# Optimization experiments

Hardware: AMD Instinct MI355X
Metric: run time of the kernel (lower is better)

## Reference

```python
import jax, jax.numpy as jnp
import numpy as np

T, N, E = 32, 5000, 80000
F_IN, H, HD, NH, C = 128, 128, 512, 8, 10
DH = H // NH  # head dim
EPS = 1e-5


def _gcn_conv(x, src, dst, W, b):
    n = x.shape[0]
    loops = jnp.arange(n, dtype=src.dtype)
    s = jnp.concatenate([src, loops])
    d = jnp.concatenate([dst, loops])
    deg = jax.ops.segment_sum(jnp.ones_like(d, x.dtype), d, num_segments=n)
    dinv = jnp.where(deg > 0, jax.lax.rsqrt(deg), 0.0)
    h = x @ W  # [n, H]
    norm = dinv[s] * dinv[d]  # [e]
    out = jax.ops.segment_sum(h[s] * norm[:, None], d, num_segments=n)
    return out + b


def _graph_embed(x, ei, W0, b0, W1, b1, W2, b2):
    src, dst = ei[0], ei[1]
    h = jnp.tanh(_gcn_conv(x, src, dst, W0, b0))
    h = jnp.tanh(_gcn_conv(h, src, dst, W1, b1))
    h = jnp.tanh(_gcn_conv(h, src, dst, W2, b2))
    return jnp.sum(h, axis=0)  # SumAggregation over all nodes -> [H]


def _forward(x, edge_index, W0, b0, W1, b1, W2, b2,
             Wq, bq, Wk, bk, Wv, bv, Wo, bo,
             g2, beta2, Wm1, bm1, Wm2, bm2, Wl, bl):
    # per-graph GCN stack + sum aggregation -> [T, H]
    z = jax.vmap(_graph_embed, in_axes=(0, 0) + (None,) * 6)(
        x, edge_index, W0, b0, W1, b1, W2, b2)

    # unbatched multihead self-attention over the T sequence
    q = (z @ Wq + bq).reshape(T, NH, DH)
    k = (z @ Wk + bk).reshape(T, NH, DH)
    v = (z @ Wv + bv).reshape(T, NH, DH)
    scores = jnp.einsum('thd,shd->hts', q, k) / jnp.sqrt(jnp.asarray(DH, z.dtype))
    attn = jax.nn.softmax(scores, axis=-1)
    o = jnp.einsum('hts,shd->thd', attn, v).reshape(T, H)
    x_attend = o @ Wo + bo  # dropout1 is identity in eval
    # NOTE: layer_norm1 output is dead code in the original forward (assigned to x, never used)

    mlp = jax.nn.relu(x_attend @ Wm1 + bm1) @ Wm2 + bm2
    x_attend = x_attend + mlp  # dropout2 identity in eval

    mu = jnp.mean(x_attend, axis=-1, keepdims=True)
    var = jnp.var(x_attend, axis=-1, keepdims=True)
    x_attend = (x_attend - mu) * jax.lax.rsqrt(var + EPS) * g2 + beta2

    pooled = jnp.sum(jax.nn.relu(x_attend), axis=0)  # [H]
    return pooled @ Wl + bl  # [C]


def setup_inputs() -> dict:
    key = jax.random.key(0)
    ks = jax.random.split(key, 24)

    def lin(k, fan_in, shape):
        return jax.random.normal(k, shape, jnp.float32) / np.sqrt(fan_in)

    inp = {
        'x': jax.random.normal(ks[0], (T, N, F_IN), jnp.float32),
        'edge_index': jax.random.randint(ks[1], (T, 2, E), 0, N, jnp.int32),
        'W0': lin(ks[2], F_IN, (F_IN, H)), 'b0': jnp.zeros((H,), jnp.float32),
        'W1': lin(ks[3], H, (H, H)), 'b1': jnp.zeros((H,), jnp.float32),
        'W2': lin(ks[4], H, (H, H)), 'b2': jnp.zeros((H,), jnp.float32),
        'Wq': lin(ks[5], H, (H, H)), 'bq': jnp.zeros((H,), jnp.float32),
        'Wk': lin(ks[6], H, (H, H)), 'bk': jnp.zeros((H,), jnp.float32),
        'Wv': lin(ks[7], H, (H, H)), 'bv': jnp.zeros((H,), jnp.float32),
        'Wo': lin(ks[8], H, (H, H)), 'bo': jnp.zeros((H,), jnp.float32),
        'g2': jnp.ones((H,), jnp.float32), 'beta2': jnp.zeros((H,), jnp.float32),
        'Wm1': lin(ks[9], H, (H, HD)), 'bm1': jnp.zeros((HD,), jnp.float32),
        'Wm2': lin(ks[10], HD, (HD, H)), 'bm2': jnp.zeros((H,), jnp.float32),
        'Wl': lin(ks[11], H, (H, C)), 'bl': jnp.zeros((C,), jnp.float32),
    }
    return inp


def reference(x, edge_index, W0, b0, W1, b1, W2, b2,
              Wq, bq, Wk, bk, Wv, bv, Wo, bo,
              g2, beta2, Wm1, bm1, Wm2, bm2, Wl, bl):
    return _forward(x, edge_index, W0, b0, W1, b1, W2, b2,
                    Wq, bq, Wk, bk, Wv, bv, Wo, bo,
                    g2, beta2, Wm1, bm1, Wm2, bm2, Wl, bl)
```

## Files before the change

### kernel.cpp

```cpp
#include <hip/hip_runtime.h>
#include <cstdint>

#define T_ 32
#define N_ 5000
#define E_ 80000
#define H_ 128
#define HD_ 512
#define C_ 10

typedef _Float16 f16;
typedef f16 f16x8 __attribute__((ext_vector_type(8)));
typedef f16 f16x4 __attribute__((ext_vector_type(4)));
typedef f16 f16x2 __attribute__((ext_vector_type(2)));
typedef float f32x4 __attribute__((ext_vector_type(4)));

#define LDA 136
#define LDH 136
#define NB_ 8
#define EPS_ (E_ / NB_)
#define NBLK_ 313
#define GEMMB 768

__device__ inline float fast_tanh(float x) {
    return 1.0f - 2.0f / (__expf(2.0f * x) + 1.0f);
}

__device__ inline f16x8 cvt8(float4 a, float4 b) {
    return (f16x8){(f16)a.x, (f16)a.y, (f16)a.z, (f16)a.w,
                   (f16)b.x, (f16)b.y, (f16)b.z, (f16)b.w};
}

__global__ __launch_bounds__(256) void k_count(const int* __restrict__ ei, int* __restrict__ part) {
    __shared__ int cnt[N_];
    int blk = blockIdx.x;
    int t = blk & 31, seg = blk >> 5;
    int tid = threadIdx.x;
    for (int i = tid; i < N_; i += 256) cnt[i] = 0;
    __syncthreads();
    const int* dst = ei + (size_t)t * 2 * E_ + E_ + seg * EPS_;
    for (int e = tid * 4; e < EPS_; e += 1024) {
        int4 d = *(const int4*)&dst[e];
        atomicAdd(&cnt[d.x], 1);
        atomicAdd(&cnt[d.y], 1);
        atomicAdd(&cnt[d.z], 1);
        atomicAdd(&cnt[d.w], 1);
    }
    __syncthreads();
    int* p = part + (t * NB_ + seg) * N_;
    for (int i = tid * 4; i < N_; i += 1024) *(int4*)&p[i] = *(const int4*)&cnt[i];
}

__global__ __launch_bounds__(256) void k_scan(int* __restrict__ part, int* __restrict__ ptr,
                                              float* __restrict__ dinv, float* __restrict__ z) {
    __shared__ int cnt[N_];
    __shared__ int red[256];
    int t = blockIdx.x, tid = threadIdx.x;
    int base = t * N_;
    if (tid < 128) z[t * 128 + tid] = 0.0f;
    int* pp = part + t * NB_ * N_;

    for (int i = tid; i < N_; i += 256) {
        int c = 0;
#pragma unroll
        for (int s = 0; s < NB_; ++s) c += pp[s * N_ + i];
        cnt[i] = c;
        dinv[base + i] = rsqrtf((float)(c + 1));
    }
    __syncthreads();

    int vals[20];
    int sum = 0;
#pragma unroll
    for (int j = 0; j < 20; ++j) {
        int i = tid * 20 + j;
        int c = (i < N_) ? cnt[i] : 0;
        vals[j] = sum;
        sum += c;
    }
    red[tid] = sum;
    __syncthreads();
    for (int off = 1; off < 256; off <<= 1) {
        int v = (tid >= off) ? red[tid - off] : 0;
        __syncthreads();
        red[tid] += v;
        __syncthreads();
    }
    int prev = (tid > 0) ? red[tid - 1] : 0;
#pragma unroll
    for (int j = 0; j < 20; ++j) {
        int i = tid * 20 + j;
        if (i < N_) cnt[i] = prev + vals[j];
    }
    __syncthreads();

    for (int i = tid; i < N_; i += 256) {
        int run = cnt[i];
        ptr[base + i] = run;
#pragma unroll
        for (int s = 0; s < NB_; ++s) {
            int c = pp[s * N_ + i];
            pp[s * N_ + i] = run;
            run += c;
        }
    }
}

__global__ __launch_bounds__(256) void k_scatter(const int* __restrict__ ei,
                                                 const int* __restrict__ part,
                                                 uint16_t* __restrict__ col) {
    __shared__ int cur[N_];
    int blk = blockIdx.x;
    int t = blk & 31, seg = blk >> 5;
    int tid = threadIdx.x;
    const int* off = part + (t * NB_ + seg) * N_;
    for (int i = tid * 4; i < N_; i += 1024) *(int4*)&cur[i] = *(const int4*)&off[i];
    __syncthreads();
    const int* src = ei + (size_t)t * 2 * E_ + seg * EPS_;
    const int* dst = src + E_;
    uint16_t* cl = col + (size_t)t * E_;
    for (int e = tid * 4; e < EPS_; e += 1024) {
        int4 s4 = *(const int4*)&src[e];
        int4 d4 = *(const int4*)&dst[e];
        cl[atomicAdd(&cur[d4.x], 1)] = (uint16_t)s4.x;
        cl[atomicAdd(&cur[d4.y], 1)] = (uint16_t)s4.y;
        cl[atomicAdd(&cur[d4.z], 1)] = (uint16_t)s4.z;
        cl[atomicAdd(&cur[d4.w], 1)] = (uint16_t)s4.w;
    }
}

__global__ __launch_bounds__(256) void k_wprep(const float* __restrict__ W0,
                                               const float* __restrict__ W1,
                                               const float* __restrict__ W2,
                                               f16* __restrict__ Wt) {
    const float* W = (blockIdx.x == 0) ? W0 : (blockIdx.x == 1) ? W1 : W2;
    f16* dst = Wt + blockIdx.x * 16384;
    for (int idx = threadIdx.x; idx < 16384; idx += 256) {
        int c = idx >> 7, k = idx & 127;
        dst[idx] = (f16)W[k * 128 + c];
    }
}

template <bool F32IN>
__global__ __launch_bounds__(256, 3) void k_gemm(const void* __restrict__ in_,
                                                 const f16* __restrict__ Wt,
                                                 const float* __restrict__ dinv,
                                                 f16* __restrict__ g) {
    __shared__ f16 Ws[128 * LDA];
    __shared__ f16 slab[4][16 * LDA];
    int tid = threadIdx.x;
    {
        int c = tid >> 1, hf = tid & 1;
        const f16* src = Wt + c * 128 + hf * 64;
        f16* dst = Ws + c * LDA + hf * 64;
#pragma unroll
        for (int j = 0; j < 8; ++j) *(f16x8*)&dst[j * 8] = *(const f16x8*)&src[j * 8];
    }
    __syncthreads();

    int xc = blockIdx.x & 7;
    int jb = blockIdx.x >> 3;
    int w = tid >> 6, lane = tid & 63;
    int m = lane & 15, q = lane >> 4;
    int co = q * 8;
    f16* sl = slab[w];
    int srow = lane >> 4;
    int scol = (lane & 15) * 8;

    for (int task = jb * 4 + w; task < 4 * NBLK_; task += 384) {
        int gsel = task / NBLK_;
        int tile = task - gsel * NBLK_;
        int t = xc + (gsel << 3);
        int base = t * N_;
        int r0 = tile * 16;
        int rowA = r0 + m; if (rowA >= N_) rowA = N_ - 1;

        f16x8 a0, a1, a2, a3;
        if (F32IN) {
            const float* src = (const float*)in_ + (((size_t)(base + rowA)) << 7) + co;
            float4 u0 = *(const float4*)&src[0];
            float4 u1 = *(const float4*)&src[4];
            float4 u2 = *(const float4*)&src[32];
            float4 u3 = *(const float4*)&src[36];
            float4 u4 = *(const float4*)&src[64];
            float4 u5 = *(const float4*)&src[68];
            float4 u6 = *(const float4*)&src[96];
            float4 u7 = *(const float4*)&src[100];
            a0 = cvt8(u0, u1); a1 = cvt8(u2, u3); a2 = cvt8(u4, u5); a3 = cvt8(u6, u7);
        } else {
            const f16* src = (const f16*)in_ + (((size_t)(base + rowA)) << 7) + co;
            a0 = *(const f16x8*)&src[0];
            a1 = *(const f16x8*)&src[32];
            a2 = *(const f16x8*)&src[64];
            a3 = *(const f16x8*)&src[96];
        }

        f32x4 acc[8];
#pragma unroll
        for (int n = 0; n < 8; ++n) acc[n] = (f32x4){0.f, 0.f, 0.f, 0.f};
#pragma unroll
        for (int n = 0; n < 8; ++n) {
            f16x8 bF = *(const f16x8*)&Ws[(n * 16 + m) * LDA + co];
            acc[n] = __builtin_amdgcn_mfma_f32_16x16x32_f16(a0, bF, acc[n], 0, 0, 0);
        }
#pragma unroll
        for (int n = 0; n < 8; ++n) {
            f16x8 bF = *(const f16x8*)&Ws[(n * 16 + m) * LDA + 32 + co];
            acc[n] = __builtin_amdgcn_mfma_f32_16x16x32_f16(a1, bF, acc[n], 0, 0, 0);
        }
#pragma unroll
        for (int n = 0; n < 8; ++n) {
            f16x8 bF = *(const f16x8*)&Ws[(n * 16 + m) * LDA + 64 + co];
            acc[n] = __builtin_amdgcn_mfma_f32_16x16x32_f16(a2, bF, acc[n], 0, 0, 0);
        }
#pragma unroll
        for (int n = 0; n < 8; ++n) {
            f16x8 bF = *(const f16x8*)&Ws[(n * 16 + m) * LDA + 96 + co];
            acc[n] = __builtin_amdgcn_mfma_f32_16x16x32_f16(a3, bF, acc[n], 0, 0, 0);
        }

#pragma unroll
        for (int i = 0; i < 4; ++i) {
            int rr = q * 4 + i;
            int gr = r0 + rr; if (gr >= N_) gr = N_ - 1;
            float d = dinv[base + gr];
#pragma unroll
            for (int n = 0; n < 8; ++n)
                sl[rr * LDA + n * 16 + m] = (f16)(acc[n][i] * d);
        }
        asm volatile("s_waitcnt lgkmcnt(0)" ::: "memory");
#pragma unroll
        for (int j4 = 0; j4 < 4; ++j4) {
            int row = j4 * 4 + srow;
            f16x8 v = *(const f16x8*)&sl[row * LDA + scol];
            if (r0 + row < N_)
                *(f16x8*)&g[(((size_t)(base + r0 + row)) << 7) + scol] = v;
        }
    }
}

__global__ __launch_bounds__(256, 3) void k_fused(const int* __restrict__ ptr,
                                                  const uint16_t* __restrict__ col,
                                                  const f16* __restrict__ g,
                                                  const float* __restrict__ dinv,
                                                  const float* __restrict__ b,
                                                  const f16* __restrict__ Wn,
                                                  int zbase,
                                                  f16* __restrict__ out) {
    __shared__ f16 hs[16 * LDH];
    __shared__ f16 ot[16 * LDH];
    int x = blockIdx.x & 7;
    int j = blockIdx.x >> 3;
    int gsel = j / NBLK_;
    int nb = j - gsel * NBLK_;
    int t = x + (gsel << 3);

    int tid = threadIdx.x;
    int w = tid >> 6;
    int lane = tid & 63;
    int q = lane >> 4, m = lane & 15;
    int base = t * N_;
    const f16* gg = g + (size_t)base * H_;
    const uint16_t* cl = col + (size_t)t * E_;
    int r0 = nb * 16;
    int n0 = r0 + w * 4;
    if (n0 > N_ - 4) n0 = N_ - 4;
    int n = n0 + q;
    unsigned moB = (unsigned)(m * 8);

    int4 p4 = *(const int4*)&ptr[base + n0];
    int pend = (n0 + 4 < N_) ? ptr[base + n0 + 4] : E_;
    int begin = (q == 0) ? p4.x : (q == 1) ? p4.y : (q == 2) ? p4.z : p4.w;
    int end   = (q == 0) ? p4.y : (q == 1) ? p4.z : (q == 2) ? p4.w : pend;

    float dn = dinv[base + n];
    float4 b4a = *(const float4*)&b[m * 8];
    float4 b4b = *(const float4*)&b[m * 8 + 4];

    int zidx = zbase - 5000 * t;

    f16x8 a0 = *(const f16x8*)&gg[((unsigned)n << 7) + moB];
    f16x8 a1 = {}, a2 = {}, a3 = {}, a4 = {}, a5 = {}, a6 = {}, a7 = {};

    int e0 = begin & ~7;
    int elast = (end - 1) & ~7;
    unsigned span = (unsigned)(end - begin);
    uint4 cc = *(const uint4*)&cl[e0];
    for (int e = e0; e < end; e += 8) {
        int en = e + 8;
        int epf = en < elast ? en : elast;
        uint4 cn = *(const uint4*)&cl[epf];
        unsigned eb = (unsigned)(e - begin);
        int i0 = (int)(cc.x & 0xFFFFu), i1 = (int)(cc.x >> 16);
        int i2 = (int)(cc.y & 0xFFFFu), i3 = (int)(cc.y >> 16);
        int i4 = (int)(cc.z & 0xFFFFu), i5 = (int)(cc.z >> 16);
        int i6 = (int)(cc.w & 0xFFFFu), i7 = (int)(cc.w >> 16);
        int s0 = (eb + 0 < span) ? i0 : zidx;
        int s1 = (eb + 1 < span) ? i1 : zidx;
        int s2 = (eb + 2 < span) ? i2 : zidx;
        int s3 = (eb + 3 < span) ? i3 : zidx;
        int s4 = (eb + 4 < span) ? i4 : zidx;
        int s5 = (eb + 5 < span) ? i5 : zidx;
        int s6 = (eb + 6 < span) ? i6 : zidx;
        int s7 = (eb + 7 < span) ? i7 : zidx;
        f16x8 v0 = *(const f16x8*)&gg[((unsigned)s0 << 7) + moB];
        f16x8 v1 = *(const f16x8*)&gg[((unsigned)s1 << 7) + moB];
        f16x8 v2 = *(const f16x8*)&gg[((unsigned)s2 << 7) + moB];
        f16x8 v3 = *(const f16x8*)&gg[((unsigned)s3 << 7) + moB];
        f16x8 v4 = *(const f16x8*)&gg[((unsigned)s4 << 7) + moB];
        f16x8 v5 = *(const f16x8*)&gg[((unsigned)s5 << 7) + moB];
        f16x8 v6 = *(const f16x8*)&gg[((unsigned)s6 << 7) + moB];
        f16x8 v7 = *(const f16x8*)&gg[((unsigned)s7 << 7) + moB];
        a0 += v0; a1 += v1; a2 += v2; a3 += v3;
        a4 += v4; a5 += v5; a6 += v6; a7 += v7;
        cc = cn;
    }
    a0 += a1; a2 += a3; a4 += a5; a6 += a7;
    a0 += a2; a4 += a6;
    a0 += a4;

    f16x8 o;
#pragma unroll
    for (int jj = 0; jj < 8; ++jj) {
        float bj = (jj < 4) ? ((const float*)&b4a)[jj] : ((const float*)&b4b)[jj - 4];
        o[jj] = (f16)fast_tanh(dn * (float)a0[jj] + bj);
    }
    *(f16x8*)&hs[(w * 4 + q) * LDH + m * 8] = o;
    __syncthreads();

    f32x4 acc0 = (f32x4){0.f, 0.f, 0.f, 0.f};
    f32x4 acc1 = (f32x4){0.f, 0.f, 0.f, 0.f};
#pragma unroll
    for (int kb = 0; kb < 4; ++kb) {
        f16x8 aF = *(const f16x8*)&hs[m * LDH + kb * 32 + q * 8];
        f16x8 b0F = *(const f16x8*)&Wn[(w * 32 + m) * 128 + kb * 32 + q * 8];
        f16x8 b1F = *(const f16x8*)&Wn[(w * 32 + 16 + m) * 128 + kb * 32 + q * 8];
        acc0 = __builtin_amdgcn_mfma_f32_16x16x32_f16(aF, b0F, acc0, 0, 0, 0);
        acc1 = __builtin_amdgcn_mfma_f32_16x16x32_f16(aF, b1F, acc1, 0, 0, 0);
    }
#pragma unroll
    for (int i = 0; i < 4; ++i) {
        int rr = q * 4 + i;
        int gr = r0 + rr; if (gr >= N_) gr = N_ - 1;
        float d = dinv[base + gr];
        ot[rr * LDH + w * 32 + m]      = (f16)(acc0[i] * d);
        ot[rr * LDH + w * 32 + 16 + m] = (f16)(acc1[i] * d);
    }
    __syncthreads();
    {
        int row = tid >> 4, c8 = (tid & 15) * 8;
        if (r0 + row < N_) {
            f16x8 v = *(const f16x8*)&ot[row * LDH + c8];
            *(f16x8*)&out[((size_t)(base + r0 + row)) * H_ + c8] = v;
        }
    }
}

__global__ __launch_bounds__(256) void k_aggr(const int* __restrict__ ptr,
                                              const uint16_t* __restrict__ col,
                                              const f16* __restrict__ g,
                                              const float* __restrict__ dinv,
                                              const float* __restrict__ b,
                                              f16* __restrict__ out) {
    int x = blockIdx.x & 7;
    int j = blockIdx.x >> 3;
    int gsel = j / NBLK_;
    int nb = j - gsel * NBLK_;
    int t = x + (gsel << 3);

    int w = threadIdx.x >> 6;
    int lane = threadIdx.x & 63;
    int q = lane >> 4, m = lane & 15;
    int n0 = nb * 16 + w * 4;
    if (n0 >= N_) return;
    int base = t * N_;
    const f16* gg = g + (size_t)base * H_;
    const uint16_t* cl = col + (size_t)t * E_;
    int n = n0 + q;
    unsigned moB = (unsigned)(m * 8);

    int4 p4 = *(const int4*)&ptr[base + n0];
    int pend = (n0 + 4 < N_) ? ptr[base + n0 + 4] : E_;
    int begin = (q == 0) ? p4.x : (q == 1) ? p4.y : (q == 2) ? p4.z : p4.w;
    int end   = (q == 0) ? p4.y : (q == 1) ? p4.z : (q == 2) ? p4.w : pend;

    float dn = dinv[base + n];
    float4 b4a = *(const float4*)&b[m * 8];
    float4 b4b = *(const float4*)&b[m * 8 + 4];

    int zidx = 320000 - 5000 * t;

    f16x8 a0 = *(const f16x8*)&gg[((unsigned)n << 7) + moB];
    f16x8 a1 = {}, a2 = {}, a3 = {}, a4 = {}, a5 = {}, a6 = {}, a7 = {};

    int e0 = begin & ~7;
    int elast = (end - 1) & ~7;
    unsigned span = (unsigned)(end - begin);
    uint4 cc = *(const uint4*)&cl[e0];
    for (int e = e0; e < end; e += 8) {
        int en = e + 8;
        int epf = en < elast ? en : elast;
        uint4 cn = *(const uint4*)&cl[epf];
        unsigned eb = (unsigned)(e - begin);
        int i0 = (int)(cc.x & 0xFFFFu), i1 = (int)(cc.x >> 16);
        int i2 = (int)(cc.y & 0xFFFFu), i3 = (int)(cc.y >> 16);
        int i4 = (int)(cc.z & 0xFFFFu), i5 = (int)(cc.z >> 16);
        int i6 = (int)(cc.w & 0xFFFFu), i7 = (int)(cc.w >> 16);
        int s0 = (eb + 0 < span) ? i0 : zidx;
        int s1 = (eb + 1 < span) ? i1 : zidx;
        int s2 = (eb + 2 < span) ? i2 : zidx;
        int s3 = (eb + 3 < span) ? i3 : zidx;
        int s4 = (eb + 4 < span) ? i4 : zidx;
        int s5 = (eb + 5 < span) ? i5 : zidx;
        int s6 = (eb + 6 < span) ? i6 : zidx;
        int s7 = (eb + 7 < span) ? i7 : zidx;
        f16x8 v0 = *(const f16x8*)&gg[((unsigned)s0 << 7) + moB];
        f16x8 v1 = *(const f16x8*)&gg[((unsigned)s1 << 7) + moB];
        f16x8 v2 = *(const f16x8*)&gg[((unsigned)s2 << 7) + moB];
        f16x8 v3 = *(const f16x8*)&gg[((unsigned)s3 << 7) + moB];
        f16x8 v4 = *(const f16x8*)&gg[((unsigned)s4 << 7) + moB];
        f16x8 v5 = *(const f16x8*)&gg[((unsigned)s5 << 7) + moB];
        f16x8 v6 = *(const f16x8*)&gg[((unsigned)s6 << 7) + moB];
        f16x8 v7 = *(const f16x8*)&gg[((unsigned)s7 << 7) + moB];
        a0 += v0; a1 += v1; a2 += v2; a3 += v3;
        a4 += v4; a5 += v5; a6 += v6; a7 += v7;
        cc = cn;
    }
    a0 += a1; a2 += a3; a4 += a5; a6 += a7;
    a0 += a2; a4 += a6;
    a0 += a4;

    f16x8 o;
#pragma unroll
    for (int jj = 0; jj < 8; ++jj) {
        float bj = (jj < 4) ? ((const float*)&b4a)[jj] : ((const float*)&b4b)[jj - 4];
        o[jj] = (f16)fast_tanh(dn * (float)a0[jj] + bj);
    }
    *(f16x8*)&out[((size_t)base + n) * H_ + moB] = o;
}

__global__ __launch_bounds__(256) void k_reduce(const f16* __restrict__ h, float* __restrict__ z) {
    int t = blockIdx.x, seg = blockIdx.y;
    int tid = threadIdx.x;
    int rg = tid >> 5;
    int c = (tid & 31) * 4;
    const f16* p = h + (size_t)t * N_ * H_;
    float4 acc = make_float4(0.f, 0.f, 0.f, 0.f);
    int n0 = seg * 500;
    for (int n = n0 + rg; n < n0 + 500; n += 8) {
        f16x4 v = *(const f16x4*)&p[(size_t)n * H_ + c];
        acc.x += (float)v[0]; acc.y += (float)v[1]; acc.z += (float)v[2]; acc.w += (float)v[3];
    }
    __shared__ float4 part[256];
    part[tid] = acc;
    __syncthreads();
    if (rg == 0) {
        float4 s = part[tid];
#pragma unroll
        for (int j = 1; j < 8; ++j) {
            float4 v = part[(j << 5) + tid];
            s.x += v.x; s.y += v.y; s.z += v.z; s.w += v.w;
        }
        atomicAdd(&z[t * H_ + c + 0], s.x);
        atomicAdd(&z[t * H_ + c + 1], s.y);
        atomicAdd(&z[t * H_ + c + 2], s.z);
        atomicAdd(&z[t * H_ + c + 3], s.w);
    }
}

__global__ __launch_bounds__(128) void k_qkv(const float* __restrict__ z,
                                             const float* __restrict__ Wq, const float* __restrict__ bq,
                                             const float* __restrict__ Wk, const float* __restrict__ bk,
                                             const float* __restrict__ Wv, const float* __restrict__ bv,
                                             float* __restrict__ q, float* __restrict__ k,
                                             float* __restrict__ v) {
    int t = blockIdx.x, c = threadIdx.x;
    __shared__ float zs[128];
    zs[c] = z[t * 128 + c];
    __syncthreads();
    float aq = bq[c], ak = bk[c], av = bv[c];
    for (int kk = 0; kk < 128; ++kk) {
        float zv = zs[kk];
        aq += zv * Wq[(kk << 7) + c];
        ak += zv * Wk[(kk << 7) + c];
        av += zv * Wv[(kk << 7) + c];
    }
    q[t * 128 + c] = aq;
    k[t * 128 + c] = ak;
    v[t * 128 + c] = av;
}

__global__ __launch_bounds__(256) void k_attnmid(
    const float* __restrict__ q, const float* __restrict__ k, const float* __restrict__ v,
    const float* __restrict__ Wo, const float* __restrict__ bo,
    const float* __restrict__ g2, const float* __restrict__ beta2,
    const float* __restrict__ Wm1, const float* __restrict__ bm1,
    const float* __restrict__ Wm2, const float* __restrict__ bm2,
    float* __restrict__ xr) {
    int t = blockIdx.x, tid = threadIdx.x;
    __shared__ float Ks[32 * 128], Vs[32 * 128];
    __shared__ float qs[128], sc[8 * 32], xa[128], hid[512], ys[128];
    __shared__ float redA[128], redB[128];

    for (int i = tid; i < 32 * 128; i += 256) { Ks[i] = k[i]; Vs[i] = v[i]; }
    if (tid < 128) qs[tid] = q[t * 128 + tid];
    __syncthreads();

    {
        int h = tid >> 5, s = tid & 31;
        float d = 0.0f;
#pragma unroll
        for (int kk = 0; kk < 16; ++kk)
            d += qs[(h << 4) + kk] * Ks[(s << 7) + (h << 4) + kk];
        sc[tid] = d * 0.25f;
    }
    __syncthreads();
    if (tid < 8) {
        float m = -1e30f;
        for (int s = 0; s < 32; ++s) m = fmaxf(m, sc[(tid << 5) + s]);
        float l = 0.0f;
        for (int s = 0; s < 32; ++s) { float e = __expf(sc[(tid << 5) + s] - m); sc[(tid << 5) + s] = e; l += e; }
        float inv = 1.0f / l;
        for (int s = 0; s < 32; ++s) sc[(tid << 5) + s] *= inv;
    }
    __syncthreads();
    if (tid < 128) {
        int h = tid >> 4;
        float o = 0.0f;
        for (int s = 0; s < 32; ++s) o += sc[(h << 5) + s] * Vs[(s << 7) + tid];
        qs[tid] = o;
    }
    __syncthreads();
    if (tid < 128) {
        float a = bo[tid];
        for (int kk = 0; kk < 128; ++kk) a += qs[kk] * Wo[(kk << 7) + tid];
        xa[tid] = a;
    }
    __syncthreads();
    for (int j = tid; j < 512; j += 256) {
        float a = bm1[j];
        for (int kk = 0; kk < 128; ++kk) a += xa[kk] * Wm1[(kk << 9) + j];
        hid[j] = fmaxf(a, 0.0f);
    }
    __syncthreads();
    if (tid < 128) {
        float a = bm2[tid];
        for (int j = 0; j < 512; ++j) a += hid[j] * Wm2[(j << 7) + tid];
        ys[tid] = xa[tid] + a;
    }
    __syncthreads();
    if (tid < 128) { redA[tid] = ys[tid]; redB[tid] = ys[tid] * ys[tid]; }
    __syncthreads();
    for (int off = 64; off > 0; off >>= 1) {
        if (tid < off) { redA[tid] += redA[tid + off]; redB[tid] += redB[tid + off]; }
        __syncthreads();
    }
    float mu = redA[0] * (1.0f / 128.0f);
    float var = redB[0] * (1.0f / 128.0f) - mu * mu;
    float rs = rsqrtf(var + 1e-5f);
    if (tid < 128) {
        float yv = (ys[tid] - mu) * rs * g2[tid] + beta2[tid];
        xr[t * 128 + tid] = fmaxf(yv, 0.0f);
    }
}

__global__ __launch_bounds__(128) void k_final(const float* __restrict__ xr,
                                               const float* __restrict__ Wl,
                                               const float* __restrict__ bl,
                                               float* __restrict__ out) {
    int tid = threadIdx.x;
    __shared__ float pooled[128];
    float s = 0.0f;
    for (int t = 0; t < 32; ++t) s += xr[t * 128 + tid];
    pooled[tid] = s;
    __syncthreads();
    if (tid < C_) {
        float a = bl[tid];
        for (int kk = 0; kk < 128; ++kk) a += pooled[kk] * Wl[kk * C_ + tid];
        out[tid] = a;
    }
}

extern "C" void kernel_launch(void* const* d_in, const int* in_sizes, int n_in,
                              void* d_out, int out_size, void* d_ws, size_t ws_size,
                              hipStream_t stream) {
    const float* x  = (const float*)d_in[0];
    const int*   ei = (const int*)d_in[1];
    const float* W0 = (const float*)d_in[2];  const float* b0 = (const float*)d_in[3];
    const float* W1 = (const float*)d_in[4];  const float* b1 = (const float*)d_in[5];
    const float* W2 = (const float*)d_in[6];  const float* b2 = (const float*)d_in[7];
    const float* Wq = (const float*)d_in[8];  const float* bq = (const float*)d_in[9];
    const float* Wk = (const float*)d_in[10]; const float* bk = (const float*)d_in[11];
    const float* Wv = (const float*)d_in[12]; const float* bv = (const float*)d_in[13];
    const float* Wo = (const float*)d_in[14]; const float* bo = (const float*)d_in[15];
    const float* g2 = (const float*)d_in[16]; const float* beta2 = (const float*)d_in[17];
    const float* Wm1 = (const float*)d_in[18]; const float* bm1 = (const float*)d_in[19];
    const float* Wm2 = (const float*)d_in[20]; const float* bm2 = (const float*)d_in[21];
    const float* Wl = (const float*)d_in[22]; const float* bl = (const float*)d_in[23];
    float* outp = (float*)d_out;

    const size_t BIG = (size_t)T_ * N_ * H_;
    char* ws = (char*)d_ws;
    float*    dinv = (float*)(ws);
    int*      ptr  = (int*)(ws + 640000);
    uint16_t* col  = (uint16_t*)(ws + 1280000);
    f16*      Wt   = (f16*)(ws + 6400000);
    f16*      P16  = (f16*)(ws + 6498304);
    f16*      Q16  = P16 + BIG;
    float*    z    = (float*)(Q16 + BIG);
    float*    zq   = z + 4096;
    float*    zk   = zq + 4096;
    float*    zv   = zk + 4096;
    float*    xr   = zv + 4096;
    int*      part = (int*)P16;

    k_wprep<<<3, 256, 0, stream>>>(W0, W1, W2, Wt);
    k_count<<<NB_ * 32, 256, 0, stream>>>(ei, part);
    k_scan<<<T_, 256, 0, stream>>>(part, ptr, dinv, z);
    k_scatter<<<NB_ * 32, 256, 0, stream>>>(ei, part, col);

    const int AGGR_BLOCKS = NBLK_ * 32;
    k_gemm<true><<<GEMMB, 256, 0, stream>>>(x, Wt, dinv, P16);
    k_fused<<<AGGR_BLOCKS, 256, 0, stream>>>(ptr, col, P16, dinv, b0, Wt + 16384, 320000, Q16);
    k_fused<<<AGGR_BLOCKS, 256, 0, stream>>>(ptr, col, Q16, dinv, b1, Wt + 32768, 160000, P16);
    k_aggr<<<AGGR_BLOCKS, 256, 0, stream>>>(ptr, col, P16, dinv, b2, Q16);

    k_reduce<<<dim3(T_, 10), 256, 0, stream>>>(Q16, z);

    k_qkv<<<T_, 128, 0, stream>>>(z, Wq, bq, Wk, bk, Wv, bv, zq, zk, zv);
    k_attnmid<<<T_, 256, 0, stream>>>(zq, zk, zv, Wo, bo, g2, beta2,
                                      Wm1, bm1, Wm2, bm2, xr);
    k_final<<<1, 128, 0, stream>>>(xr, Wl, bl, outp);
}
```

Measured before the change: 526.4 us.

## Split fused aggregate+GEMM into separate kernels and fuse final sum-reduction into aggregation

Removes the k_fused kernel that did neighbour aggregation plus a per-block 16-row MFMA transform, and replaces it with plain aggregation kernels followed by standalone k_gemm<false> launches for layers 1 and 2. The last layer's aggregation now reduces tanh outputs across the wave with shuffles and atomically adds into z, so the separate k_reduce pass and its full write and re-read of the activation buffer go away. The zero-row index used for padded edges moves to a dedicated zeroed region past z. Two extra kernel launches and extra round-trips of intermediate buffers are added in exchange for higher occupancy in aggregation and a more efficient GEMM.

```diff
diff --git a/kernel.cpp b/kernel.cpp
--- a/kernel.cpp
+++ b/kernel.cpp
@@ -15,11 +15,11 @@
 typedef float f32x4 __attribute__((ext_vector_type(4)));
 
 #define LDA 136
-#define LDH 136
 #define NB_ 8
 #define EPS_ (E_ / NB_)
 #define NBLK_ 313
 #define GEMMB 768
+#define ZROW_ 320064
 
 __device__ inline float fast_tanh(float x) {
     return 1.0f - 2.0f / (__expf(2.0f * x) + 1.0f);
@@ -57,6 +57,7 @@
     int t = blockIdx.x, tid = threadIdx.x;
     int base = t * N_;
     if (tid < 128) z[t * 128 + tid] = 0.0f;
+    if (tid >= 128 && tid < 192) z[4096 + (tid - 128)] = 0.0f;
     int* pp = part + t * NB_ * N_;
 
     for (int i = tid; i < N_; i += 256) {
@@ -238,32 +239,26 @@
     }
 }
 
-__global__ __launch_bounds__(256, 3) void k_fused(const int* __restrict__ ptr,
-                                                  const uint16_t* __restrict__ col,
-                                                  const f16* __restrict__ g,
-                                                  const float* __restrict__ dinv,
-                                                  const float* __restrict__ b,
-                                                  const f16* __restrict__ Wn,
-                                                  int zbase,
-                                                  f16* __restrict__ out) {
-    __shared__ f16 hs[16 * LDH];
-    __shared__ f16 ot[16 * LDH];
+__global__ __launch_bounds__(256) void k_aggr(const int* __restrict__ ptr,
+                                              const uint16_t* __restrict__ col,
+                                              const f16* __restrict__ g,
+                                              const float* __restrict__ dinv,
+                                              const float* __restrict__ b,
+                                              f16* __restrict__ out) {
     int x = blockIdx.x & 7;
     int j = blockIdx.x >> 3;
     int gsel = j / NBLK_;
     int nb = j - gsel * NBLK_;
     int t = x + (gsel << 3);
 
-    int tid = threadIdx.x;
-    int w = tid >> 6;
-    int lane = tid & 63;
+    int w = threadIdx.x >> 6;
+    int lane = threadIdx.x & 63;
     int q = lane >> 4, m = lane & 15;
+    int n0 = nb * 16 + w * 4;
+    if (n0 >= N_) return;
     int base = t * N_;
     const f16* gg = g + (size_t)base * H_;
     const uint16_t* cl = col + (size_t)t * E_;
-    int r0 = nb * 16;
-    int n0 = r0 + w * 4;
-    if (n0 > N_ - 4) n0 = N_ - 4;
     int n = n0 + q;
     unsigned moB = (unsigned)(m * 8);
 
@@ -276,7 +271,7 @@
     float4 b4a = *(const float4*)&b[m * 8];
     float4 b4b = *(const float4*)&b[m * 8 + 4];
 
-    int zidx = zbase - 5000 * t;
+    int zidx = ZROW_ - 5000 * t;
 
     f16x8 a0 = *(const f16x8*)&gg[((unsigned)n << 7) + moB];
     f16x8 a1 = {}, a2 = {}, a3 = {}, a4 = {}, a5 = {}, a6 = {}, a7 = {};
@@ -324,43 +319,15 @@
         float bj = (jj < 4) ? ((const float*)&b4a)[jj] : ((const float*)&b4b)[jj - 4];
         o[jj] = (f16)fast_tanh(dn * (float)a0[jj] + bj);
     }
-    *(f16x8*)&hs[(w * 4 + q) * LDH + m * 8] = o;
-    __syncthreads();
-
-    f32x4 acc0 = (f32x4){0.f, 0.f, 0.f, 0.f};
-    f32x4 acc1 = (f32x4){0.f, 0.f, 0.f, 0.f};
-#pragma unroll
-    for (int kb = 0; kb < 4; ++kb) {
-        f16x8 aF = *(const f16x8*)&hs[m * LDH + kb * 32 + q * 8];
-        f16x8 b0F = *(const f16x8*)&Wn[(w * 32 + m) * 128 + kb * 32 + q * 8];
-        f16x8 b1F = *(const f16x8*)&Wn[(w * 32 + 16 + m) * 128 + kb * 32 + q * 8];
-        acc0 = __builtin_amdgcn_mfma_f32_16x16x32_f16(aF, b0F, acc0, 0, 0, 0);
-        acc1 = __builtin_amdgcn_mfma_f32_16x16x32_f16(aF, b1F, acc1, 0, 0, 0);
-    }
-#pragma unroll
-    for (int i = 0; i < 4; ++i) {
-        int rr = q * 4 + i;
-        int gr = r0 + rr; if (gr >= N_) gr = N_ - 1;
-        float d = dinv[base + gr];
-        ot[rr * LDH + w * 32 + m]      = (f16)(acc0[i] * d);
-        ot[rr * LDH + w * 32 + 16 + m] = (f16)(acc1[i] * d);
-    }
-    __syncthreads();
-    {
-        int row = tid >> 4, c8 = (tid & 15) * 8;
-        if (r0 + row < N_) {
-            f16x8 v = *(const f16x8*)&ot[row * LDH + c8];
-            *(f16x8*)&out[((size_t)(base + r0 + row)) * H_ + c8] = v;
-        }
-    }
-}
-
-__global__ __launch_bounds__(256) void k_aggr(const int* __restrict__ ptr,
-                                              const uint16_t* __restrict__ col,
-                                              const f16* __restrict__ g,
-                                              const float* __restrict__ dinv,
-                                              const float* __restrict__ b,
-                                              f16* __restrict__ out) {
+    *(f16x8*)&out[((size_t)base + n) * H_ + moB] = o;
+}
+
+__global__ __launch_bounds__(256) void k_aggr_red(const int* __restrict__ ptr,
+                                                  const uint16_t* __restrict__ col,
+                                                  const f16* __restrict__ g,
+                                                  const float* __restrict__ dinv,
+                                                  const float* __restrict__ b,
+                                                  float* __restrict__ z) {
     int x = blockIdx.x & 7;
     int j = blockIdx.x >> 3;
     int gsel = j / NBLK_;
@@ -387,7 +354,7 @@
     float4 b4a = *(const float4*)&b[m * 8];
     float4 b4b = *(const float4*)&b[m * 8 + 4];
 
-    int zidx = 320000 - 5000 * t;
+    int zidx = ZROW_ - 5000 * t;
 
     f16x8 a0 = *(const f16x8*)&gg[((unsigned)n << 7) + moB];
     f16x8 a1 = {}, a2 = {}, a3 = {}, a4 = {}, a5 = {}, a6 = {}, a7 = {};
@@ -429,41 +396,35 @@
     a0 += a2; a4 += a6;
     a0 += a4;
 
-    f16x8 o;
-#pragma unroll
-    for (int jj = 0; jj < 8; ++jj) {
-        float bj = (jj < 4) ? ((const float*)&b4a)[jj] : ((const float*)&b4b)[jj - 4];
-        o[jj] = (f16)fast_tanh(dn * (float)a0[jj] + bj);
-    }
-    *(f16x8*)&out[((size_t)base + n) * H_ + moB] = o;
-}
-
-__global__ __launch_bounds__(256) void k_reduce(const f16* __restrict__ h, float* __restrict__ z) {
-    int t = blockIdx.x, seg = blockIdx.y;
-    int tid = threadIdx.x;
-    int rg = tid >> 5;
-    int c = (tid & 31) * 4;
-    const f16* p = h + (size_t)t * N_ * H_;
-    float4 acc = make_float4(0.f, 0.f, 0.f, 0.f);
-    int n0 = seg * 500;
-    for (int n = n0 + rg; n < n0 + 500; n += 8) {
-        f16x4 v = *(const f16x4*)&p[(size_t)n * H_ + c];
-        acc.x += (float)v[0]; acc.y += (float)v[1]; acc.z += (float)v[2]; acc.w += (float)v[3];
-    }
-    __shared__ float4 part[256];
-    part[tid] = acc;
-    __syncthreads();
-    if (rg == 0) {
-        float4 s = part[tid];
-#pragma unroll
-        for (int j = 1; j < 8; ++j) {
-            float4 v = part[(j << 5) + tid];
-            s.x += v.x; s.y += v.y; s.z += v.z; s.w += v.w;
-        }
-        atomicAdd(&z[t * H_ + c + 0], s.x);
-        atomicAdd(&z[t * H_ + c + 1], s.y);
-        atomicAdd(&z[t * H_ + c + 2], s.z);
-        atomicAdd(&z[t * H_ + c + 3], s.w);
+    float s0_, s1_, s2_, s3_, s4_, s5_, s6_, s7_;
+    {
+        float bj0 = ((const float*)&b4a)[0], bj1 = ((const float*)&b4a)[1];
+        float bj2 = ((const float*)&b4a)[2], bj3 = ((const float*)&b4a)[3];
+        float bj4 = ((const float*)&b4b)[0], bj5 = ((const float*)&b4b)[1];
+        float bj6 = ((const float*)&b4b)[2], bj7 = ((const float*)&b4b)[3];
+        s0_ = (float)(f16)fast_tanh(dn * (float)a0[0] + bj0);
+        s1_ = (float)(f16)fast_tanh(dn * (float)a0[1] + bj1);
+        s2_ = (float)(f16)fast_tanh(dn * (float)a0[2] + bj2);
+        s3_ = (float)(f16)fast_tanh(dn * (float)a0[3] + bj3);
+        s4_ = (float)(f16)fast_tanh(dn * (float)a0[4] + bj4);
+        s5_ = (float)(f16)fast_tanh(dn * (float)a0[5] + bj5);
+        s6_ = (float)(f16)fast_tanh(dn * (float)a0[6] + bj6);
+        s7_ = (float)(f16)fast_tanh(dn * (float)a0[7] + bj7);
+    }
+    s0_ += __shfl_xor(s0_, 16, 64); s0_ += __shfl_xor(s0_, 32, 64);
+    s1_ += __shfl_xor(s1_, 16, 64); s1_ += __shfl_xor(s1_, 32, 64);
+    s2_ += __shfl_xor(s2_, 16, 64); s2_ += __shfl_xor(s2_, 32, 64);
+    s3_ += __shfl_xor(s3_, 16, 64); s3_ += __shfl_xor(s3_, 32, 64);
+    s4_ += __shfl_xor(s4_, 16, 64); s4_ += __shfl_xor(s4_, 32, 64);
+    s5_ += __shfl_xor(s5_, 16, 64); s5_ += __shfl_xor(s5_, 32, 64);
+    s6_ += __shfl_xor(s6_, 16, 64); s6_ += __shfl_xor(s6_, 32, 64);
+    s7_ += __shfl_xor(s7_, 16, 64); s7_ += __shfl_xor(s7_, 32, 64);
+    if (q == 0) {
+        float* zp = z + t * 128 + m * 8;
+        atomicAdd(&zp[0], s0_); atomicAdd(&zp[1], s1_);
+        atomicAdd(&zp[2], s2_); atomicAdd(&zp[3], s3_);
+        atomicAdd(&zp[4], s4_); atomicAdd(&zp[5], s5_);
+        atomicAdd(&zp[6], s6_); atomicAdd(&zp[7], s7_);
     }
 }
 
@@ -607,7 +568,7 @@
     f16*      P16  = (f16*)(ws + 6498304);
     f16*      Q16  = P16 + BIG;
     float*    z    = (float*)(Q16 + BIG);
-    float*    zq   = z + 4096;
+    float*    zq   = z + 4096 + 64;
     float*    zk   = zq + 4096;
     float*    zv   = zk + 4096;
     float*    xr   = zv + 4096;
@@ -620,11 +581,11 @@
 
     const int AGGR_BLOCKS = NBLK_ * 32;
     k_gemm<true><<<GEMMB, 256, 0, stream>>>(x, Wt, dinv, P16);
-    k_fused<<<AGGR_BLOCKS, 256, 0, stream>>>(ptr, col, P16, dinv, b0, Wt + 16384, 320000, Q16);
-    k_fused<<<AGGR_BLOCKS, 256, 0, stream>>>(ptr, col, Q16, dinv, b1, Wt + 32768, 160000, P16);
-    k_aggr<<<AGGR_BLOCKS, 256, 0, stream>>>(ptr, col, P16, dinv, b2, Q16);
-
-    k_reduce<<<dim3(T_, 10), 256, 0, stream>>>(Q16, z);
+    k_aggr<<<AGGR_BLOCKS, 256, 0, stream>>>(ptr, col, P16, dinv, b0, Q16);
+    k_gemm<false><<<GEMMB, 256, 0, stream>>>(Q16, Wt + 16384, dinv, P16);
+    k_aggr<<<AGGR_BLOCKS, 256, 0, stream>>>(ptr, col, P16, dinv, b1, Q16);
+    k_gemm<false><<<GEMMB, 256, 0, stream>>>(Q16, Wt + 32768, dinv, P16);
+    k_aggr_red<<<AGGR_BLOCKS, 256, 0, stream>>>(ptr, col, P16, dinv, b2, z);
 
     k_qkv<<<T_, 128, 0, stream>>>(z, Wq, bq, Wk, bk, Wv, bv, zq, zk, zv);
     k_attnmid<<<T_, 256, 0, stream>>>(zq, zk, zv, Wo, bo, g2, beta2,
```

After: 1.362 ms. +158.7%, slower.
